# Performance work log

Hardware: AMD Instinct MI355X
Metric: run time of the kernel (lower is better)

Reference implementation:

```python
import jax, jax.numpy as jnp
import numpy as np

EPS = 1e-7
LN_EPS = 1e-6


def project(x):
    norm = jnp.maximum(jnp.linalg.norm(x, axis=-1, keepdims=True), EPS)
    max_norm = 1.0 - EPS
    return jnp.where(norm >= 1.0, x / norm * max_norm, x)


def mobius_add(x, y, c):
    x2 = jnp.sum(x * x, -1, keepdims=True)
    y2 = jnp.sum(y * y, -1, keepdims=True)
    xy = jnp.sum(x * y, -1, keepdims=True)
    num = (1 + 2 * c * xy + c * y2) * x + (1 - c * x2) * y
    den = 1 + 2 * c * xy + c * c * x2 * y2
    return project(num / jnp.maximum(den, EPS))


def logmap0(y, c):
    sqrt_c = jnp.maximum(jnp.sqrt(c), EPS)
    y_norm = jnp.linalg.norm(y, axis=-1, keepdims=True)
    safe = jnp.maximum(y_norm, EPS)
    mag = jnp.arctanh(jnp.minimum(y_norm, 1.0 - EPS)) / sqrt_c
    return jnp.where(y_norm < EPS, jnp.zeros_like(y), mag * (y / safe))


def expmap0(v, c):
    sqrt_c = jnp.maximum(jnp.sqrt(c), EPS)
    v_norm = jnp.linalg.norm(v, axis=-1, keepdims=True)
    safe = jnp.maximum(v_norm, EPS)
    mag = jnp.tanh(sqrt_c * safe) / sqrt_c
    return project(jnp.where(v_norm < EPS, jnp.zeros_like(v), mag * (v / safe)))


def poincare_dist(x, y, c):
    # x: [B,H,N,1,D], y: [B,H,N,W,D], c: [B,1,1,1,1] -> dist [B,H,N,W]
    sqrt_c = jnp.maximum(jnp.sqrt(c), EPS)
    add_norm = jnp.linalg.norm(mobius_add(-x, y, c), axis=-1)
    arg = jnp.minimum(sqrt_c.squeeze(-1) * add_norm, 1.0 - EPS)
    return 2.0 * jnp.arctanh(arg) / sqrt_c.squeeze(-1)


def sliding_windows(x, window):
    # x: [B,H,N,Dh] -> [B,H,N,window,Dh] of the last `window` keys per query (zero-padded)
    B, H, N, Dh = x.shape
    pad = jnp.zeros((B, H, window - 1, Dh), dtype=x.dtype)
    xp = jnp.concatenate([pad, x], axis=2)
    idx = jnp.arange(window)[None, :] + jnp.arange(N)[:, None]  # [N, W]
    return xp[:, :, idx, :]


def layer_norm(x, scale, bias):
    mu = jnp.mean(x, axis=-1, keepdims=True)
    var = jnp.mean(jnp.square(x - mu), axis=-1, keepdims=True)
    return (x - mu) * jax.lax.rsqrt(var + LN_EPS) * scale + bias


def setup_inputs() -> dict:
    key = jax.random.key(0)
    B, N, DIM, H = 2, 1024, 1024, 16
    Dh = DIM // H
    ks = jax.random.split(key, 16)
    s = 1.0 / np.sqrt(DIM)
    x = 0.01 * jax.random.normal(ks[0], (B, N, DIM), jnp.float32)  # well inside the ball
    # rotary angles: pos * inv_freq, shape [N, Dh//2]
    inv_freq = 1.0 / (10000.0 ** (np.arange(0, Dh // 2, dtype=np.float32) * 2.0 / Dh))
    freqs = jnp.asarray(np.arange(N, dtype=np.float32)[:, None] * inv_freq[None, :])
    c = 0.5 + 0.5 * jax.random.uniform(ks[1], (B,), jnp.float32)
    p = {
        'Wq': s * jax.random.normal(ks[2], (DIM, DIM), jnp.float32), 'bq': jnp.zeros((DIM,), jnp.float32),
        'Wk': s * jax.random.normal(ks[3], (DIM, DIM), jnp.float32), 'bk': jnp.zeros((DIM,), jnp.float32),
        'Wv': s * jax.random.normal(ks[4], (DIM, DIM), jnp.float32), 'bv': jnp.zeros((DIM,), jnp.float32),
        'Wo': s * jax.random.normal(ks[5], (DIM, DIM), jnp.float32), 'bo': jnp.zeros((DIM,), jnp.float32),
        'W1': s * jax.random.normal(ks[6], (DIM, 4 * DIM), jnp.float32), 'b1': jnp.zeros((4 * DIM,), jnp.float32),
        'W2': (1.0 / np.sqrt(4 * DIM)) * jax.random.normal(ks[7], (4 * DIM, DIM), jnp.float32), 'b2': jnp.zeros((DIM,), jnp.float32),
        'ln1_scale': jnp.ones((DIM,), jnp.float32), 'ln1_bias': jnp.zeros((DIM,), jnp.float32),
        'ln2_scale': jnp.ones((DIM,), jnp.float32), 'ln2_bias': jnp.zeros((DIM,), jnp.float32),
        'geo_scale': jnp.ones((H, 1, 1), jnp.float32),
    }
    return dict(x=x, freqs=freqs, c=c, **p)


def reference(x, freqs, c, Wq, bq, Wk, bk, Wv, bv, Wo, bo, W1, b1, W2, b2,
              ln1_scale, ln1_bias, ln2_scale, ln2_bias, geo_scale):
    WINDOW = 32
    B, N, DIM = x.shape
    H = geo_scale.shape[0]
    Dh = DIM // H
    c_ln = c.reshape(B, 1, 1)
    c_attn = c.reshape(B, 1, 1, 1)
    c_d = c.reshape(B, 1, 1, 1, 1)

    # tangent-space layer norm 1
    x_norm = expmap0(layer_norm(logmap0(x, c_ln), ln1_scale, ln1_bias), c_ln)
    x_tan = logmap0(x_norm, c_ln)

    q = (x_tan @ Wq + bq).reshape(B, N, H, Dh)
    k = (x_tan @ Wk + bk).reshape(B, N, H, Dh)
    v = (x_tan @ Wv + bv).reshape(B, N, H, Dh)

    # rotary embedding (real-arithmetic form of complex multiply)
    cos = jnp.cos(freqs).reshape(1, N, 1, Dh // 2)
    sin = jnp.sin(freqs).reshape(1, N, 1, Dh // 2)

    def rope(t):
        t_r, t_i = jnp.split(t, 2, -1)
        return jnp.concatenate([t_r * cos - t_i * sin, t_r * sin + t_i * cos], -1)

    q_hyp = expmap0(rope(q), c_attn)
    k_hyp = expmap0(rope(k), c_attn)

    q_t = q_hyp.transpose(0, 2, 1, 3)  # [B,H,N,Dh]
    k_t = k_hyp.transpose(0, 2, 1, 3)
    v_t = v.transpose(0, 2, 1, 3)

    k_w = sliding_windows(k_t, WINDOW)  # [B,H,N,W,Dh]
    v_w = sliding_windows(v_t, WINDOW)

    dist = poincare_dist(q_t[:, :, :, None, :], k_w, c_d)  # [B,H,N,W]
    attn = jax.nn.softmax(-geo_scale * dist, axis=-1)
    attn_out = jnp.einsum('bhnw,bhnwd->bhnd', attn, v_w).transpose(0, 2, 1, 3).reshape(B, N, DIM)

    attn_hyp = expmap0(attn_out @ Wo + bo, c_ln)
    x_att = mobius_add(x, attn_hyp, c_ln)

    # tangent-space layer norm 2 + hyperbolic FFN
    x_norm2 = expmap0(layer_norm(logmap0(x_att, c_ln), ln2_scale, ln2_bias), c_ln)
    t = logmap0(x_norm2, c_ln)
    ffn_tan = jax.nn.gelu(t @ W1 + b1) @ W2 + b2
    x_ffn = expmap0(ffn_tan, c_ln)
    return mobius_add(x_att, x_ffn, c_ln)
```

## Files before the change

### kernel.cpp

```cpp
#include <hip/hip_runtime.h>
#include <cmath>

static constexpr int SEQ = 1024;
static constexpr int DIM = 1024;
static constexpr int NH  = 16;
static constexpr int DH  = 64;
static constexpr int WB  = 2;
static constexpr int ROWS = WB * SEQ;
__device__ static constexpr double D_EPS = 1e-7;

typedef __attribute__((ext_vector_type(8))) short short8v;
typedef __attribute__((ext_vector_type(4))) float float4v;

__device__ __forceinline__ uint32_t bf16_hi_bits(float f) {
  uint32_t u = __float_as_uint(f);
  return (u + 0x7fffu + ((u >> 16) & 1u)) >> 16;
}
__device__ __forceinline__ uint32_t pack_hl(float f) {
  const uint32_t h = bf16_hi_bits(f);
  const float fh = __uint_as_float(h << 16);
  const uint32_t l = bf16_hi_bits(f - fh);
  return h | (l << 16);
}

__device__ __forceinline__ double wsum64(double v) {
#pragma unroll
  for (int m = 32; m >= 1; m >>= 1) v += __shfl_xor(v, m, 64);
  return v;
}

__global__ __launch_bounds__(256) void ln_tan_kernel(
    const float* __restrict__ xin, const float* __restrict__ cb,
    const float* __restrict__ gamma, const float* __restrict__ beta,
    uint32_t* __restrict__ out) {
  __shared__ double sh[2][4];
  const int row = blockIdx.x;
  const int b = row / SEQ;
  const float* xr = xin + (size_t)row * DIM;
  const int t = threadIdx.x;
  float xv[4];
  double s0 = 0.0, s1 = 0.0;
#pragma unroll
  for (int i = 0; i < 4; i++) {
    xv[i] = xr[t + 256 * i];
    s0 += (double)xv[i];
    s1 += (double)xv[i] * (double)xv[i];
  }
  s0 = wsum64(s0); s1 = wsum64(s1);
  const int wid = t >> 6, lane = t & 63;
  if (lane == 0) { sh[0][wid] = s0; sh[1][wid] = s1; }
  __syncthreads();
  s0 = sh[0][0] + sh[0][1] + sh[0][2] + sh[0][3];
  s1 = sh[1][0] + sh[1][1] + sh[1][2] + sh[1][3];

  const double cc  = (double)cb[b];
  const double sqc = fmax(sqrt(cc), D_EPS);
  const double xn  = sqrt(s1);
  double a = 0.0;
  if (xn >= D_EPS) a = atanh(fmin(xn, 1.0 - D_EPS)) / sqc / fmax(xn, D_EPS);
  const double mu   = a * s0 / (double)DIM;
  const double var  = a * a * s1 / (double)DIM - mu * mu;
  const double invs = 1.0 / sqrt(var + 1e-6);

  double tv[4]; double s2 = 0.0;
#pragma unroll
  for (int i = 0; i < 4; i++) {
    const int col = t + 256 * i;
    tv[i] = (a * (double)xv[i] - mu) * invs * (double)gamma[col] + (double)beta[col];
    s2 += tv[i] * tv[i];
  }
  s2 = wsum64(s2);
  __syncthreads();
  if (lane == 0) sh[0][wid] = s2;
  __syncthreads();
  s2 = sh[0][0] + sh[0][1] + sh[0][2] + sh[0][3];

  const double tn = sqrt(s2);
  double C = 0.0;
  if (tn >= D_EPS) {
    const double safe_t = fmax(tn, D_EPS);
    const double mag2 = tanh(sqc * safe_t) / sqc;
    const double en = mag2 * (tn / safe_t);
    const double pn = fmax(en, D_EPS);
    const double f  = (pn >= 1.0) ? (1.0 - D_EPS) / pn : 1.0;
    const double yn = en * f;
    if (yn >= D_EPS) {
      const double mag3 = atanh(fmin(yn, 1.0 - D_EPS)) / sqc;
      C = (mag2 / safe_t) * f * (mag3 / fmax(yn, D_EPS));
    }
  }
  uint32_t* orow = out + (size_t)row * DIM;
#pragma unroll
  for (int i = 0; i < 4; i++) orow[t + 256 * i] = pack_hl((float)(tv[i] * C));
}

__global__ __launch_bounds__(256) void expmobius_parts4_kernel(
    const float* __restrict__ xb, const float* __restrict__ parts,
    const float* __restrict__ bias, const float* __restrict__ cb,
    float* __restrict__ out) {
  __shared__ double sh[3][4];
  const size_t PSZ = (size_t)ROWS * DIM;
  const int row = blockIdx.x;
  const int b = row / SEQ;
  const float* xr = xb + (size_t)row * DIM;
  const float* p0r = parts + (size_t)row * DIM;
  const int t = threadIdx.x;
  float xv[4];
  double tv[4];
  double sx2 = 0.0, st2 = 0.0, sxt = 0.0;
#pragma unroll
  for (int i = 0; i < 4; i++) {
    const int col = t + 256 * i;
    xv[i] = xr[col];
    tv[i] = (double)p0r[col] + (double)p0r[col + PSZ] +
            (double)p0r[col + 2 * PSZ] + (double)p0r[col + 3 * PSZ] +
            (double)bias[col];
    sx2 += (double)xv[i] * (double)xv[i];
    st2 += tv[i] * tv[i];
    sxt += (double)xv[i] * tv[i];
  }
  sx2 = wsum64(sx2); st2 = wsum64(st2); sxt = wsum64(sxt);
  const int wid = t >> 6, lane = t & 63;
  if (lane == 0) { sh[0][wid] = sx2; sh[1][wid] = st2; sh[2][wid] = sxt; }
  __syncthreads();
  sx2 = sh[0][0] + sh[0][1] + sh[0][2] + sh[0][3];
  st2 = sh[1][0] + sh[1][1] + sh[1][2] + sh[1][3];
  sxt = sh[2][0] + sh[2][1] + sh[2][2] + sh[2][3];

  const double cc  = (double)cb[b];
  const double sqc = fmax(sqrt(cc), D_EPS);
  const double tn = sqrt(st2);
  double s = 0.0;
  if (tn >= D_EPS) {
    const double safe = fmax(tn, D_EPS);
    const double mag = tanh(sqc * safe) / sqc;
    const double en = mag * (tn / safe);
    const double pn = fmax(en, D_EPS);
    const double f  = (pn >= 1.0) ? (1.0 - D_EPS) / pn : 1.0;
    s = (mag / safe) * f;
  }
  const double x2 = sx2, y2 = s * s * st2, xy = s * sxt;
  const double P   = 1.0 + 2.0 * cc * xy + cc * y2;
  const double Q   = 1.0 - cc * x2;
  const double den = fmax(1.0 + 2.0 * cc * xy + cc * cc * x2 * y2, D_EPS);
  const double num2 = P * P * x2 + Q * Q * y2 + 2.0 * P * Q * xy;
  const double rn  = sqrt(fmax(num2, 0.0)) / den;
  const double pn2 = fmax(rn, D_EPS);
  const double pf  = (pn2 >= 1.0) ? (1.0 - D_EPS) / pn2 : 1.0;
  const double Pd = (P / den) * pf;
  const double Qd = (Q / den) * pf * s;
  float* orow = out + (size_t)row * DIM;
#pragma unroll
  for (int i = 0; i < 4; i++)
    orow[t + 256 * i] = (float)(Pd * (double)xv[i] + Qd * tv[i]);
}

__global__ __launch_bounds__(256) void rope_expmap_kernel(
    float* __restrict__ q, float* __restrict__ k,
    const float* __restrict__ freqs, const float* __restrict__ cb) {
  const int row = blockIdx.x;
  const int b = row / SEQ, n = row % SEQ;
  const int t = threadIdx.x;
  const int h = t >> 4, j = t & 15;
  const int p1 = j, p2 = j + 16;
  const double f1 = (double)freqs[n * (DH / 2) + p1];
  const double f2 = (double)freqs[n * (DH / 2) + p2];
  const double c1 = cos(f1), s1 = sin(f1);
  const double c2 = cos(f2), s2 = sin(f2);
  const double cc  = (double)cb[b];
  const double sqc = fmax(sqrt(cc), D_EPS);
  const size_t base = (size_t)row * DIM + (size_t)h * DH;
  float* arrs[2] = {q, k};
#pragma unroll
  for (int a = 0; a < 2; a++) {
    float* p = arrs[a] + base;
    const double xr1 = p[p1], xi1 = p[p1 + 32];
    const double xr2 = p[p2], xi2 = p[p2 + 32];
    const double r1 = xr1 * c1 - xi1 * s1, i1 = xr1 * s1 + xi1 * c1;
    const double r2 = xr2 * c2 - xi2 * s2, i2 = xr2 * s2 + xi2 * c2;
    double nrm2 = r1 * r1 + i1 * i1 + r2 * r2 + i2 * i2;
#pragma unroll
    for (int m = 8; m >= 1; m >>= 1) nrm2 += __shfl_xor(nrm2, m, 16);
    const double vn = sqrt(nrm2);
    double sc = 0.0;
    if (vn >= D_EPS) {
      const double safe = fmax(vn, D_EPS);
      const double mag = tanh(sqc * safe) / sqc;
      const double en = mag * (vn / safe);
      const double pn = fmax(en, D_EPS);
      const double f  = (pn >= 1.0) ? (1.0 - D_EPS) / pn : 1.0;
      sc = (mag / safe) * f;
    }
    p[p1] = (float)(r1 * sc); p[p1 + 32] = (float)(i1 * sc);
    p[p2] = (float)(r2 * sc); p[p2 + 32] = (float)(i2 * sc);
  }
}

__global__ __launch_bounds__(256) void attn_kernel(
    const float* __restrict__ qh, const float* __restrict__ kh,
    const float* __restrict__ v, const float* __restrict__ cb,
    const float* __restrict__ geo, uint32_t* __restrict__ out) {
  __shared__ float qs[8][DH];
  const int g = threadIdx.x >> 5;
  const int w = threadIdx.x & 31;
  const int gid = blockIdx.x * 8 + g;
  const int n = gid & (SEQ - 1);
  const int bh = gid >> 10;
  const int h = bh & (NH - 1);
  const int b = bh >> 4;
  const size_t qbase = ((size_t)(b * SEQ + n)) * DIM + (size_t)h * DH;
  qs[g][w] = qh[qbase + w];
  qs[g][w + 32] = qh[qbase + w + 32];
  __syncthreads();

  const double cc  = (double)cb[b];
  const double sqc = fmax(sqrt(cc), D_EPS);
  double q2p = (double)qs[g][w] * qs[g][w] + (double)qs[g][w + 32] * qs[g][w + 32];
#pragma unroll
  for (int m = 16; m >= 1; m >>= 1) q2p += __shfl_xor(q2p, m, 32);
  const double a2 = q2p;

  const int msrc = n - 31 + w;
  double y2 = 0.0, qy = 0.0;
  if (msrc >= 0) {
    const float* kr = kh + ((size_t)(b * SEQ + msrc)) * DIM + (size_t)h * DH;
#pragma unroll 8
    for (int d = 0; d < DH; d++) {
      const double kv = (double)kr[d];
      y2 += kv * kv;
      qy += (double)qs[g][d] * kv;
    }
  }
  const double ay = -qy;
  const double P = 1.0 + 2.0 * cc * ay + cc * y2;
  const double Q = 1.0 - cc * a2;
  const double den = fmax(1.0 + 2.0 * cc * ay + cc * cc * a2 * y2, D_EPS);
  const double num2 = P * P * a2 + Q * Q * y2 + 2.0 * P * Q * ay;
  const double rn = sqrt(fmax(num2, 0.0)) / den;
  const double pn = fmax(rn, D_EPS);
  const double addn = (pn >= 1.0) ? (1.0 - D_EPS) * (rn / pn) : rn;
  const double arg = fmin(sqc * addn, 1.0 - D_EPS);
  const double dist = 2.0 * atanh(arg) / sqc;
  const double logit = -(double)geo[h] * dist;

  double mx = logit;
#pragma unroll
  for (int m = 16; m >= 1; m >>= 1) mx = fmax(mx, __shfl_xor(mx, m, 32));
  const double e = exp(logit - mx);
  double se = e;
#pragma unroll
  for (int m = 16; m >= 1; m >>= 1) se += __shfl_xor(se, m, 32);
  const double p = e / se;

  double acc1 = 0.0, acc2 = 0.0;
  for (int wp = 0; wp < 32; wp++) {
    const double pw = __shfl(p, wp, 32);
    const int mp = n - 31 + wp;
    if (mp >= 0) {
      const float* vr = v + ((size_t)(b * SEQ + mp)) * DIM + (size_t)h * DH;
      acc1 += pw * (double)vr[w];
      acc2 += pw * (double)vr[w + 32];
    }
  }
  out[qbase + w] = pack_hl((float)acc1);
  out[qbase + w + 32] = pack_hl((float)acc2);
}

__device__ __forceinline__ float gelu_tanh(float x) {
  const float x3 = x * x * x;
  return 0.5f * x * (1.0f + tanhf(0.7978845608028654f * (x + 0.044715f * x3)));
}

template <int EPI>
__device__ __forceinline__ void mfma_gemm_body(
    const uint32_t* __restrict__ Ap, int Kld,
    const float* __restrict__ Wf, const float* __restrict__ bias,
    void* __restrict__ Cout, int N, int k0, int klen, int m0, int n0) {
  __shared__ __align__(16) short AsH[4096], AsL[4096], BsH[4096], BsL[4096];
  const int t = threadIdx.x;
  const int lane = t & 63, wave = t >> 6;
  const int wm = (wave >> 1) << 6, wn = (wave & 1) << 6;
  const int am = t >> 1, akh = (t & 1) << 4;
  const uint32_t* Ag = Ap + (size_t)(m0 + am) * Kld + k0 + akh;
  const int as_ = am >> 4, ai = am & 15, aq0 = akh >> 3;
  short* awH0 = &AsH[((as_ << 6) + (aq0 << 4) + ai) << 3];
  short* awH1 = &AsH[((as_ << 6) + ((aq0 + 1) << 4) + ai) << 3];
  short* awL0 = &AsL[((as_ << 6) + (aq0 << 4) + ai) << 3];
  short* awL1 = &AsL[((as_ << 6) + ((aq0 + 1) << 4) + ai) << 3];
  const int bn = t & 127, bkg = (t >> 7) << 4;
  const float* Bg = Wf + (size_t)(k0 + bkg) * N + n0 + bn;
  const int bs = bn >> 4, bi = bn & 15, bq0 = bkg >> 3;
  short* bwH0 = &BsH[((bs << 6) + (bq0 << 4) + bi) << 3];
  short* bwH1 = &BsH[((bs << 6) + ((bq0 + 1) << 4) + bi) << 3];
  short* bwL0 = &BsL[((bs << 6) + (bq0 << 4) + bi) << 3];
  short* bwL1 = &BsL[((bs << 6) + ((bq0 + 1) << 4) + bi) << 3];

  float4v acc[4][4];
#pragma unroll
  for (int i = 0; i < 4; i++)
#pragma unroll
    for (int j = 0; j < 4; j++) acc[i][j] = (float4v){0.f, 0.f, 0.f, 0.f};

  uint32_t a[16];
  float bf[16];
  {
    const uint4* p = (const uint4*)Ag;
#pragma unroll
    for (int r = 0; r < 4; r++) { uint4 u = p[r]; a[4*r] = u.x; a[4*r+1] = u.y; a[4*r+2] = u.z; a[4*r+3] = u.w; }
#pragma unroll
    for (int r = 0; r < 16; r++) bf[r] = Bg[(size_t)r * N];
  }

  for (int kt = 0; kt < klen; kt += 32) {
    __syncthreads();
    {
      uint4 h0, l0, h1, l1;
      uint32_t* hp0 = (uint32_t*)&h0; uint32_t* lp0 = (uint32_t*)&l0;
      uint32_t* hp1 = (uint32_t*)&h1; uint32_t* lp1 = (uint32_t*)&l1;
#pragma unroll
      for (int r = 0; r < 4; r++) {
        hp0[r] = (a[2*r] & 0xffffu) | (a[2*r+1] << 16);
        lp0[r] = (a[2*r] >> 16) | (a[2*r+1] & 0xffff0000u);
        hp1[r] = (a[8+2*r] & 0xffffu) | (a[8+2*r+1] << 16);
        lp1[r] = (a[8+2*r] >> 16) | (a[8+2*r+1] & 0xffff0000u);
      }
      *(uint4*)awH0 = h0; *(uint4*)awL0 = l0;
      *(uint4*)awH1 = h1; *(uint4*)awL1 = l1;
    }
    {
      uint32_t hb[16], lb[16];
#pragma unroll
      for (int r = 0; r < 16; r++) {
        const uint32_t h = bf16_hi_bits(bf[r]);
        hb[r] = h;
        lb[r] = bf16_hi_bits(bf[r] - __uint_as_float(h << 16));
      }
      uint4 h0, l0, h1, l1;
      uint32_t* hp0 = (uint32_t*)&h0; uint32_t* lp0 = (uint32_t*)&l0;
      uint32_t* hp1 = (uint32_t*)&h1; uint32_t* lp1 = (uint32_t*)&l1;
#pragma unroll
      for (int r = 0; r < 4; r++) {
        hp0[r] = hb[2*r] | (hb[2*r+1] << 16);
        lp0[r] = lb[2*r] | (lb[2*r+1] << 16);
        hp1[r] = hb[8+2*r] | (hb[8+2*r+1] << 16);
        lp1[r] = lb[8+2*r] | (lb[8+2*r+1] << 16);
      }
      *(uint4*)bwH0 = h0; *(uint4*)bwL0 = l0;
      *(uint4*)bwH1 = h1; *(uint4*)bwL1 = l1;
    }
    __syncthreads();
    {
      const int ktn = (kt + 32 < klen) ? kt + 32 : kt;
      const uint4* p = (const uint4*)(Ag + ktn);
#pragma unroll
      for (int r = 0; r < 4; r++) { uint4 u = p[r]; a[4*r] = u.x; a[4*r+1] = u.y; a[4*r+2] = u.z; a[4*r+3] = u.w; }
      const float* bp = Bg + (size_t)ktn * N;
#pragma unroll
      for (int r = 0; r < 16; r++) bf[r] = bp[(size_t)r * N];
    }
    short8v aH[4], aL[4];
    const int ams = wm >> 4;
#pragma unroll
    for (int im = 0; im < 4; im++) {
      aH[im] = *(const short8v*)&AsH[(((ams + im) << 6) + lane) << 3];
      aL[im] = *(const short8v*)&AsL[(((ams + im) << 6) + lane) << 3];
    }
    const int bns = wn >> 4;
#pragma unroll
    for (int in_ = 0; in_ < 4; in_++) {
      const short8v bH = *(const short8v*)&BsH[(((bns + in_) << 6) + lane) << 3];
      const short8v bL = *(const short8v*)&BsL[(((bns + in_) << 6) + lane) << 3];
#pragma unroll
      for (int im = 0; im < 4; im++) {
        acc[im][in_] = __builtin_amdgcn_mfma_f32_16x16x32_bf16(aH[im], bH, acc[im][in_], 0, 0, 0);
        acc[im][in_] = __builtin_amdgcn_mfma_f32_16x16x32_bf16(aH[im], bL, acc[im][in_], 0, 0, 0);
        acc[im][in_] = __builtin_amdgcn_mfma_f32_16x16x32_bf16(aL[im], bH, acc[im][in_], 0, 0, 0);
      }
    }
  }
  const int cq = lane >> 4, ci = lane & 15;
#pragma unroll
  for (int im = 0; im < 4; im++) {
    const int row = m0 + wm + im * 16 + cq * 4;
#pragma unroll
    for (int in_ = 0; in_ < 4; in_++) {
      const int col = n0 + wn + in_ * 16 + ci;
      if (EPI == 2) {
        float* C = (float*)Cout;
#pragma unroll
        for (int r = 0; r < 4; r++) C[(size_t)(row + r) * N + col] = acc[im][in_][r];
      } else {
        const float bv_ = bias[col];
        if (EPI == 0) {
          float* C = (float*)Cout;
#pragma unroll
          for (int r = 0; r < 4; r++) C[(size_t)(row + r) * N + col] = acc[im][in_][r] + bv_;
        } else {
          uint32_t* C = (uint32_t*)Cout;
#pragma unroll
          for (int r = 0; r < 4; r++)
            C[(size_t)(row + r) * N + col] = pack_hl(gelu_tanh(acc[im][in_][r] + bv_));
        }
      }
    }
  }
}

__global__ __launch_bounds__(256) void qkv_mfma(
    const uint32_t* __restrict__ Ap,
    const float* __restrict__ Wq, const float* __restrict__ bq, float* __restrict__ Cq,
    const float* __restrict__ Wk, const float* __restrict__ bk, float* __restrict__ Ck,
    const float* __restrict__ Wv, const float* __restrict__ bv, float* __restrict__ Cv) {
  const int which = blockIdx.x >> 3;
  const int n0 = (blockIdx.x & 7) << 7;
  const float* W = (which == 0) ? Wq : (which == 1) ? Wk : Wv;
  const float* bias = (which == 0) ? bq : (which == 1) ? bk : bv;
  float* C = (which == 0) ? Cq : (which == 1) ? Ck : Cv;
  mfma_gemm_body<0>(Ap, DIM, W, bias, C, DIM, 0, DIM, blockIdx.y << 7, n0);
}

__global__ __launch_bounds__(256) void ffn_up_mfma(
    const uint32_t* __restrict__ Ap, const float* __restrict__ W1,
    const float* __restrict__ b1, uint32_t* __restrict__ H) {
  mfma_gemm_body<1>(Ap, DIM, W1, b1, H, 4 * DIM, 0, DIM, blockIdx.y << 7, blockIdx.x << 7);
}

__global__ __launch_bounds__(256) void gemm_splitk_mfma(
    const uint32_t* __restrict__ Ap, int Kld, const float* __restrict__ W,
    float* __restrict__ Cbase, size_t cstride, int N, int klen) {
  mfma_gemm_body<2>(Ap, Kld, W, nullptr, Cbase + (size_t)blockIdx.z * cstride, N,
                    blockIdx.z * klen, klen, blockIdx.y << 7, blockIdx.x << 7);
}

extern "C" void kernel_launch(void* const* d_in, const int* in_sizes, int n_in,
                              void* d_out, int out_size, void* d_ws, size_t ws_size,
                              hipStream_t stream) {
  const float* x     = (const float*)d_in[0];
  const float* freqs = (const float*)d_in[1];
  const float* c     = (const float*)d_in[2];
  const float* Wq = (const float*)d_in[3];  const float* bq = (const float*)d_in[4];
  const float* Wk = (const float*)d_in[5];  const float* bk = (const float*)d_in[6];
  const float* Wv = (const float*)d_in[7];  const float* bv = (const float*)d_in[8];
  const float* Wo = (const float*)d_in[9];  const float* bo = (const float*)d_in[10];
  const float* W1 = (const float*)d_in[11]; const float* b1 = (const float*)d_in[12];
  const float* W2 = (const float*)d_in[13]; const float* b2 = (const float*)d_in[14];
  const float* g1 = (const float*)d_in[15]; const float* be1 = (const float*)d_in[16];
  const float* g2 = (const float*)d_in[17]; const float* be2 = (const float*)d_in[18];
  const float* geo = (const float*)d_in[19];
  float* out = (float*)d_out;
  float* ws = (float*)d_ws;

  const size_t SZ = (size_t)ROWS * DIM;
  uint32_t* x_tanP = (uint32_t*)(ws + 0 * SZ);
  float*    qb     = ws + 1 * SZ;
  float*    kb     = ws + 2 * SZ;
  float*    vb     = ws + 3 * SZ;
  uint32_t* attP   = (uint32_t*)(ws + 4 * SZ);
  float*    x_att  = ws + 5 * SZ;
  uint32_t* h1P    = (uint32_t*)(ws + 6 * SZ);
  float*    woP    = ws + 0 * SZ;
  float*    fdP    = ws + 1 * SZ;
  uint32_t* t2P    = (uint32_t*)(ws + 0 * SZ);

  ln_tan_kernel<<<ROWS, 256, 0, stream>>>(x, c, g1, be1, x_tanP);
  qkv_mfma<<<dim3(24, ROWS / 128), 256, 0, stream>>>(
      x_tanP, Wq, bq, qb, Wk, bk, kb, Wv, bv, vb);
  rope_expmap_kernel<<<ROWS, 256, 0, stream>>>(qb, kb, freqs, c);
  attn_kernel<<<WB * NH * SEQ / 8, 256, 0, stream>>>(qb, kb, vb, c, geo, attP);
  gemm_splitk_mfma<<<dim3(DIM / 128, ROWS / 128, 4), 256, 0, stream>>>(
      attP, DIM, Wo, woP, SZ, DIM, DIM / 4);
  expmobius_parts4_kernel<<<ROWS, 256, 0, stream>>>(x, woP, bo, c, x_att);
  ln_tan_kernel<<<ROWS, 256, 0, stream>>>(x_att, c, g2, be2, t2P);
  ffn_up_mfma<<<dim3(4 * DIM / 128, ROWS / 128), 256, 0, stream>>>(t2P, W1, b1, h1P);
  gemm_splitk_mfma<<<dim3(DIM / 128, ROWS / 128, 4), 256, 0, stream>>>(
      h1P, 4 * DIM, W2, fdP, SZ, DIM, DIM);
  expmobius_parts4_kernel<<<ROWS, 256, 0, stream>>>(x_att, fdP, b2, c, out);
  (void)in_sizes; (void)n_in; (void)out_size; (void)ws_size;
}
```

Before: 461.9 us.

## Pre-split operands into tiled hi/lo bf16 planes for direct GEMM tile loads

Weights are now converted once per call by a new kernel into separate hi/lo bf16 planes, stored in a tile-major layout that matches the shared-memory MFMA tiles. Activation producers (layer norm, attention, FFN up) write the same tiled hi/lo layout. The GEMM main loop can then copy contiguous uint4 chunks straight into LDS, with no per-tile fp32-to-bf16 splitting or strided weight loads. The cost is extra weight-conversion launches, scattered 2-byte stores from the producers, and more workspace reuse, including writing x_att into the output buffer.

```diff
diff --git a/kernel.cpp b/kernel.cpp
--- a/kernel.cpp
+++ b/kernel.cpp
@@ -9,6 +9,7 @@
 static constexpr int ROWS = WB * SEQ;
 __device__ static constexpr double D_EPS = 1e-7;
 
+typedef unsigned short ushort_t;
 typedef __attribute__((ext_vector_type(8))) short short8v;
 typedef __attribute__((ext_vector_type(4))) float float4v;
 
@@ -16,23 +17,53 @@
   uint32_t u = __float_as_uint(f);
   return (u + 0x7fffu + ((u >> 16) & 1u)) >> 16;
 }
-__device__ __forceinline__ uint32_t pack_hl(float f) {
-  const uint32_t h = bf16_hi_bits(f);
-  const float fh = __uint_as_float(h << 16);
-  const uint32_t l = bf16_hi_bits(f - fh);
-  return h | (l << 16);
+
+__device__ __forceinline__ size_t tiled_addr(int row, int col, int Kld) {
+  return ((size_t)(row >> 7) * (Kld >> 5) + (col >> 5)) * 4096
+       + (size_t)((((row >> 4) & 7) << 9) + (((col >> 3) & 3) << 7) + ((row & 15) << 3) + (col & 7));
+}
+__device__ __forceinline__ void store_hl(ushort_t* __restrict__ hi, ushort_t* __restrict__ lo,
+                                         size_t addr, float f) {
+  const uint32_t hb = bf16_hi_bits(f);
+  hi[addr] = (ushort_t)hb;
+  lo[addr] = (ushort_t)bf16_hi_bits(f - __uint_as_float(hb << 16));
 }
 
 __device__ __forceinline__ double wsum64(double v) {
 #pragma unroll
   for (int m = 32; m >= 1; m >>= 1) v += __shfl_xor(v, m, 64);
   return v;
+}
+
+__global__ __launch_bounds__(256) void conv_w_kernel(
+    const float* __restrict__ W, ushort_t* __restrict__ hi, ushort_t* __restrict__ lo,
+    int K, int N) {
+  const int tid = blockIdx.x * 256 + threadIdx.x;
+  const int n = tid % N;
+  const int k0 = (tid / N) << 3;
+  uint32_t hw[4], lw[4];
+#pragma unroll
+  for (int rp = 0; rp < 4; rp++) {
+    uint32_t h2[2], l2[2];
+#pragma unroll
+    for (int e = 0; e < 2; e++) {
+      const float f = W[(size_t)(k0 + rp * 2 + e) * N + n];
+      const uint32_t hb = bf16_hi_bits(f);
+      h2[e] = hb;
+      l2[e] = bf16_hi_bits(f - __uint_as_float(hb << 16));
+    }
+    hw[rp] = h2[0] | (h2[1] << 16);
+    lw[rp] = l2[0] | (l2[1] << 16);
+  }
+  const size_t addr = tiled_addr(n, k0, K);
+  *(uint4*)&hi[addr] = *(uint4*)hw;
+  *(uint4*)&lo[addr] = *(uint4*)lw;
 }
 
 __global__ __launch_bounds__(256) void ln_tan_kernel(
     const float* __restrict__ xin, const float* __restrict__ cb,
     const float* __restrict__ gamma, const float* __restrict__ beta,
-    uint32_t* __restrict__ out) {
+    ushort_t* __restrict__ ohi, ushort_t* __restrict__ olo) {
   __shared__ double sh[2][4];
   const int row = blockIdx.x;
   const int b = row / SEQ;
@@ -89,21 +120,23 @@
       C = (mag2 / safe_t) * f * (mag3 / fmax(yn, D_EPS));
     }
   }
-  uint32_t* orow = out + (size_t)row * DIM;
-#pragma unroll
-  for (int i = 0; i < 4; i++) orow[t + 256 * i] = pack_hl((float)(tv[i] * C));
+#pragma unroll
+  for (int i = 0; i < 4; i++) {
+    const int col = t + 256 * i;
+    store_hl(ohi, olo, tiled_addr(row, col, DIM), (float)(tv[i] * C));
+  }
 }
 
 __global__ __launch_bounds__(256) void expmobius_parts4_kernel(
-    const float* __restrict__ xb, const float* __restrict__ parts,
+    const float* __restrict__ xb,
+    const float* __restrict__ p0, const float* __restrict__ p1,
+    const float* __restrict__ p2, const float* __restrict__ p3,
     const float* __restrict__ bias, const float* __restrict__ cb,
     float* __restrict__ out) {
   __shared__ double sh[3][4];
-  const size_t PSZ = (size_t)ROWS * DIM;
   const int row = blockIdx.x;
   const int b = row / SEQ;
-  const float* xr = xb + (size_t)row * DIM;
-  const float* p0r = parts + (size_t)row * DIM;
+  const size_t ro = (size_t)row * DIM;
   const int t = threadIdx.x;
   float xv[4];
   double tv[4];
@@ -111,10 +144,9 @@
 #pragma unroll
   for (int i = 0; i < 4; i++) {
     const int col = t + 256 * i;
-    xv[i] = xr[col];
-    tv[i] = (double)p0r[col] + (double)p0r[col + PSZ] +
-            (double)p0r[col + 2 * PSZ] + (double)p0r[col + 3 * PSZ] +
-            (double)bias[col];
+    xv[i] = xb[ro + col];
+    tv[i] = (double)p0[ro + col] + (double)p1[ro + col] +
+            (double)p2[ro + col] + (double)p3[ro + col] + (double)bias[col];
     sx2 += (double)xv[i] * (double)xv[i];
     st2 += tv[i] * tv[i];
     sxt += (double)xv[i] * tv[i];
@@ -149,10 +181,9 @@
   const double pf  = (pn2 >= 1.0) ? (1.0 - D_EPS) / pn2 : 1.0;
   const double Pd = (P / den) * pf;
   const double Qd = (Q / den) * pf * s;
-  float* orow = out + (size_t)row * DIM;
 #pragma unroll
   for (int i = 0; i < 4; i++)
-    orow[t + 256 * i] = (float)(Pd * (double)xv[i] + Qd * tv[i]);
+    out[ro + t + 256 * i] = (float)(Pd * (double)xv[i] + Qd * tv[i]);
 }
 
 __global__ __launch_bounds__(256) void rope_expmap_kernel(
@@ -199,7 +230,8 @@
 __global__ __launch_bounds__(256) void attn_kernel(
     const float* __restrict__ qh, const float* __restrict__ kh,
     const float* __restrict__ v, const float* __restrict__ cb,
-    const float* __restrict__ geo, uint32_t* __restrict__ out) {
+    const float* __restrict__ geo,
+    ushort_t* __restrict__ ohi, ushort_t* __restrict__ olo) {
   __shared__ float qs[8][DH];
   const int g = threadIdx.x >> 5;
   const int w = threadIdx.x & 31;
@@ -208,7 +240,8 @@
   const int bh = gid >> 10;
   const int h = bh & (NH - 1);
   const int b = bh >> 4;
-  const size_t qbase = ((size_t)(b * SEQ + n)) * DIM + (size_t)h * DH;
+  const int row = b * SEQ + n;
+  const size_t qbase = (size_t)row * DIM + (size_t)h * DH;
   qs[g][w] = qh[qbase + w];
   qs[g][w + 32] = qh[qbase + w + 32];
   __syncthreads();
@@ -262,8 +295,9 @@
       acc2 += pw * (double)vr[w + 32];
     }
   }
-  out[qbase + w] = pack_hl((float)acc1);
-  out[qbase + w + 32] = pack_hl((float)acc2);
+  const int col = h * DH + w;
+  store_hl(ohi, olo, tiled_addr(row, col, DIM), (float)acc1);
+  store_hl(ohi, olo, tiled_addr(row, col + 32, DIM), (float)acc2);
 }
 
 __device__ __forceinline__ float gelu_tanh(float x) {
@@ -273,27 +307,17 @@
 
 template <int EPI>
 __device__ __forceinline__ void mfma_gemm_body(
-    const uint32_t* __restrict__ Ap, int Kld,
-    const float* __restrict__ Wf, const float* __restrict__ bias,
-    void* __restrict__ Cout, int N, int k0, int klen, int m0, int n0) {
+    const ushort_t* __restrict__ Ahi, const ushort_t* __restrict__ Alo, int Kld,
+    const ushort_t* __restrict__ Bhi, const ushort_t* __restrict__ Blo, int KB,
+    const float* __restrict__ bias, float* __restrict__ Cf,
+    ushort_t* __restrict__ Chi, ushort_t* __restrict__ Clo, int KldOut,
+    int N, int k0, int klen, int m0, int n0) {
   __shared__ __align__(16) short AsH[4096], AsL[4096], BsH[4096], BsL[4096];
   const int t = threadIdx.x;
   const int lane = t & 63, wave = t >> 6;
   const int wm = (wave >> 1) << 6, wn = (wave & 1) << 6;
-  const int am = t >> 1, akh = (t & 1) << 4;
-  const uint32_t* Ag = Ap + (size_t)(m0 + am) * Kld + k0 + akh;
-  const int as_ = am >> 4, ai = am & 15, aq0 = akh >> 3;
-  short* awH0 = &AsH[((as_ << 6) + (aq0 << 4) + ai) << 3];
-  short* awH1 = &AsH[((as_ << 6) + ((aq0 + 1) << 4) + ai) << 3];
-  short* awL0 = &AsL[((as_ << 6) + (aq0 << 4) + ai) << 3];
-  short* awL1 = &AsL[((as_ << 6) + ((aq0 + 1) << 4) + ai) << 3];
-  const int bn = t & 127, bkg = (t >> 7) << 4;
-  const float* Bg = Wf + (size_t)(k0 + bkg) * N + n0 + bn;
-  const int bs = bn >> 4, bi = bn & 15, bq0 = bkg >> 3;
-  short* bwH0 = &BsH[((bs << 6) + (bq0 << 4) + bi) << 3];
-  short* bwH1 = &BsH[((bs << 6) + ((bq0 + 1) << 4) + bi) << 3];
-  short* bwL0 = &BsL[((bs << 6) + (bq0 << 4) + bi) << 3];
-  short* bwL1 = &BsL[((bs << 6) + ((bq0 + 1) << 4) + bi) << 3];
+  const size_t abase = (size_t)(m0 >> 7) * (Kld >> 5) * 4096;
+  const size_t bbase = (size_t)(n0 >> 7) * (KB >> 5) * 4096;
 
   float4v acc[4][4];
 #pragma unroll
@@ -301,62 +325,31 @@
 #pragma unroll
     for (int j = 0; j < 4; j++) acc[i][j] = (float4v){0.f, 0.f, 0.f, 0.f};
 
-  uint32_t a[16];
-  float bf[16];
+  uint4 rah0, rah1, ral0, ral1, rbh0, rbh1, rbl0, rbl1;
   {
-    const uint4* p = (const uint4*)Ag;
-#pragma unroll
-    for (int r = 0; r < 4; r++) { uint4 u = p[r]; a[4*r] = u.x; a[4*r+1] = u.y; a[4*r+2] = u.z; a[4*r+3] = u.w; }
-#pragma unroll
-    for (int r = 0; r < 16; r++) bf[r] = Bg[(size_t)r * N];
+    const size_t at = abase + (size_t)(k0 >> 5) * 4096;
+    const size_t bt = bbase + (size_t)(k0 >> 5) * 4096;
+    rah0 = ((const uint4*)(Ahi + at))[t]; rah1 = ((const uint4*)(Ahi + at))[t + 256];
+    ral0 = ((const uint4*)(Alo + at))[t]; ral1 = ((const uint4*)(Alo + at))[t + 256];
+    rbh0 = ((const uint4*)(Bhi + bt))[t]; rbh1 = ((const uint4*)(Bhi + bt))[t + 256];
+    rbl0 = ((const uint4*)(Blo + bt))[t]; rbl1 = ((const uint4*)(Blo + bt))[t + 256];
   }
 
   for (int kt = 0; kt < klen; kt += 32) {
     __syncthreads();
-    {
-      uint4 h0, l0, h1, l1;
-      uint32_t* hp0 = (uint32_t*)&h0; uint32_t* lp0 = (uint32_t*)&l0;
-      uint32_t* hp1 = (uint32_t*)&h1; uint32_t* lp1 = (uint32_t*)&l1;
-#pragma unroll
-      for (int r = 0; r < 4; r++) {
-        hp0[r] = (a[2*r] & 0xffffu) | (a[2*r+1] << 16);
-        lp0[r] = (a[2*r] >> 16) | (a[2*r+1] & 0xffff0000u);
-        hp1[r] = (a[8+2*r] & 0xffffu) | (a[8+2*r+1] << 16);
-        lp1[r] = (a[8+2*r] >> 16) | (a[8+2*r+1] & 0xffff0000u);
-      }
-      *(uint4*)awH0 = h0; *(uint4*)awL0 = l0;
-      *(uint4*)awH1 = h1; *(uint4*)awL1 = l1;
-    }
-    {
-      uint32_t hb[16], lb[16];
-#pragma unroll
-      for (int r = 0; r < 16; r++) {
-        const uint32_t h = bf16_hi_bits(bf[r]);
-        hb[r] = h;
-        lb[r] = bf16_hi_bits(bf[r] - __uint_as_float(h << 16));
-      }
-      uint4 h0, l0, h1, l1;
-      uint32_t* hp0 = (uint32_t*)&h0; uint32_t* lp0 = (uint32_t*)&l0;
-      uint32_t* hp1 = (uint32_t*)&h1; uint32_t* lp1 = (uint32_t*)&l1;
-#pragma unroll
-      for (int r = 0; r < 4; r++) {
-        hp0[r] = hb[2*r] | (hb[2*r+1] << 16);
-        lp0[r] = lb[2*r] | (lb[2*r+1] << 16);
-        hp1[r] = hb[8+2*r] | (hb[8+2*r+1] << 16);
-        lp1[r] = lb[8+2*r] | (lb[8+2*r+1] << 16);
-      }
-      *(uint4*)bwH0 = h0; *(uint4*)bwL0 = l0;
-      *(uint4*)bwH1 = h1; *(uint4*)bwL1 = l1;
-    }
+    ((uint4*)AsH)[t] = rah0; ((uint4*)AsH)[t + 256] = rah1;
+    ((uint4*)AsL)[t] = ral0; ((uint4*)AsL)[t + 256] = ral1;
+    ((uint4*)BsH)[t] = rbh0; ((uint4*)BsH)[t + 256] = rbh1;
+    ((uint4*)BsL)[t] = rbl0; ((uint4*)BsL)[t + 256] = rbl1;
     __syncthreads();
     {
       const int ktn = (kt + 32 < klen) ? kt + 32 : kt;
-      const uint4* p = (const uint4*)(Ag + ktn);
-#pragma unroll
-      for (int r = 0; r < 4; r++) { uint4 u = p[r]; a[4*r] = u.x; a[4*r+1] = u.y; a[4*r+2] = u.z; a[4*r+3] = u.w; }
-      const float* bp = Bg + (size_t)ktn * N;
-#pragma unroll
-      for (int r = 0; r < 16; r++) bf[r] = bp[(size_t)r * N];
+      const size_t at = abase + (size_t)((k0 + ktn) >> 5) * 4096;
+      const size_t bt = bbase + (size_t)((k0 + ktn) >> 5) * 4096;
+      rah0 = ((const uint4*)(Ahi + at))[t]; rah1 = ((const uint4*)(Ahi + at))[t + 256];
+      ral0 = ((const uint4*)(Alo + at))[t]; ral1 = ((const uint4*)(Alo + at))[t + 256];
+      rbh0 = ((const uint4*)(Bhi + bt))[t]; rbh1 = ((const uint4*)(Bhi + bt))[t + 256];
+      rbl0 = ((const uint4*)(Blo + bt))[t]; rbl1 = ((const uint4*)(Blo + bt))[t + 256];
     }
     short8v aH[4], aL[4];
     const int ams = wm >> 4;
@@ -386,50 +379,54 @@
     for (int in_ = 0; in_ < 4; in_++) {
       const int col = n0 + wn + in_ * 16 + ci;
       if (EPI == 2) {
-        float* C = (float*)Cout;
-#pragma unroll
-        for (int r = 0; r < 4; r++) C[(size_t)(row + r) * N + col] = acc[im][in_][r];
+#pragma unroll
+        for (int r = 0; r < 4; r++) Cf[(size_t)(row + r) * N + col] = acc[im][in_][r];
+      } else if (EPI == 0) {
+        const float bv_ = bias[col];
+#pragma unroll
+        for (int r = 0; r < 4; r++) Cf[(size_t)(row + r) * N + col] = acc[im][in_][r] + bv_;
       } else {
         const float bv_ = bias[col];
-        if (EPI == 0) {
-          float* C = (float*)Cout;
-#pragma unroll
-          for (int r = 0; r < 4; r++) C[(size_t)(row + r) * N + col] = acc[im][in_][r] + bv_;
-        } else {
-          uint32_t* C = (uint32_t*)Cout;
-#pragma unroll
-          for (int r = 0; r < 4; r++)
-            C[(size_t)(row + r) * N + col] = pack_hl(gelu_tanh(acc[im][in_][r] + bv_));
-        }
+#pragma unroll
+        for (int r = 0; r < 4; r++)
+          store_hl(Chi, Clo, tiled_addr(row + r, col, KldOut),
+                   gelu_tanh(acc[im][in_][r] + bv_));
       }
     }
   }
 }
 
 __global__ __launch_bounds__(256) void qkv_mfma(
-    const uint32_t* __restrict__ Ap,
-    const float* __restrict__ Wq, const float* __restrict__ bq, float* __restrict__ Cq,
-    const float* __restrict__ Wk, const float* __restrict__ bk, float* __restrict__ Ck,
-    const float* __restrict__ Wv, const float* __restrict__ bv, float* __restrict__ Cv) {
+    const ushort_t* __restrict__ Ahi, const ushort_t* __restrict__ Alo,
+    const ushort_t* __restrict__ Whi, const ushort_t* __restrict__ Wlo,
+    const float* __restrict__ bq, const float* __restrict__ bk, const float* __restrict__ bv,
+    float* __restrict__ Cq, float* __restrict__ Ck, float* __restrict__ Cv) {
   const int which = blockIdx.x >> 3;
   const int n0 = (blockIdx.x & 7) << 7;
-  const float* W = (which == 0) ? Wq : (which == 1) ? Wk : Wv;
+  const size_t woff = (size_t)which * (1u << 20);
   const float* bias = (which == 0) ? bq : (which == 1) ? bk : bv;
   float* C = (which == 0) ? Cq : (which == 1) ? Ck : Cv;
-  mfma_gemm_body<0>(Ap, DIM, W, bias, C, DIM, 0, DIM, blockIdx.y << 7, n0);
+  mfma_gemm_body<0>(Ahi, Alo, DIM, Whi + woff, Wlo + woff, DIM, bias, C,
+                    nullptr, nullptr, 0, DIM, 0, DIM, blockIdx.y << 7, n0);
 }
 
 __global__ __launch_bounds__(256) void ffn_up_mfma(
-    const uint32_t* __restrict__ Ap, const float* __restrict__ W1,
-    const float* __restrict__ b1, uint32_t* __restrict__ H) {
-  mfma_gemm_body<1>(Ap, DIM, W1, b1, H, 4 * DIM, 0, DIM, blockIdx.y << 7, blockIdx.x << 7);
+    const ushort_t* __restrict__ Ahi, const ushort_t* __restrict__ Alo,
+    const ushort_t* __restrict__ W1hi, const ushort_t* __restrict__ W1lo,
+    const float* __restrict__ b1, ushort_t* __restrict__ Hhi, ushort_t* __restrict__ Hlo) {
+  mfma_gemm_body<1>(Ahi, Alo, DIM, W1hi, W1lo, DIM, b1, nullptr, Hhi, Hlo, 4 * DIM,
+                    4 * DIM, 0, DIM, blockIdx.y << 7, blockIdx.x << 7);
 }
 
 __global__ __launch_bounds__(256) void gemm_splitk_mfma(
-    const uint32_t* __restrict__ Ap, int Kld, const float* __restrict__ W,
-    float* __restrict__ Cbase, size_t cstride, int N, int klen) {
-  mfma_gemm_body<2>(Ap, Kld, W, nullptr, Cbase + (size_t)blockIdx.z * cstride, N,
-                    blockIdx.z * klen, klen, blockIdx.y << 7, blockIdx.x << 7);
+    const ushort_t* __restrict__ Ahi, const ushort_t* __restrict__ Alo, int Kld,
+    const ushort_t* __restrict__ Bhi, const ushort_t* __restrict__ Blo, int KB,
+    float* __restrict__ C0, float* __restrict__ C1,
+    float* __restrict__ C2, float* __restrict__ C3, int N, int klen) {
+  const int z = blockIdx.z;
+  float* C = (z == 0) ? C0 : (z == 1) ? C1 : (z == 2) ? C2 : C3;
+  mfma_gemm_body<2>(Ahi, Alo, Kld, Bhi, Blo, KB, nullptr, C, nullptr, nullptr, 0,
+                    N, z * klen, klen, blockIdx.y << 7, blockIdx.x << 7);
 }
 
 extern "C" void kernel_launch(void* const* d_in, const int* in_sizes, int n_in,
@@ -451,29 +448,43 @@
   float* ws = (float*)d_ws;
 
   const size_t SZ = (size_t)ROWS * DIM;
-  uint32_t* x_tanP = (uint32_t*)(ws + 0 * SZ);
-  float*    qb     = ws + 1 * SZ;
-  float*    kb     = ws + 2 * SZ;
-  float*    vb     = ws + 3 * SZ;
-  uint32_t* attP   = (uint32_t*)(ws + 4 * SZ);
-  float*    x_att  = ws + 5 * SZ;
-  uint32_t* h1P    = (uint32_t*)(ws + 6 * SZ);
-  float*    woP    = ws + 0 * SZ;
-  float*    fdP    = ws + 1 * SZ;
-  uint32_t* t2P    = (uint32_t*)(ws + 0 * SZ);
-
-  ln_tan_kernel<<<ROWS, 256, 0, stream>>>(x, c, g1, be1, x_tanP);
+  const size_t PL = SZ;
+  const uint32_t M1 = 1u << 20;
+  auto us = [&](int i) { return (ushort_t*)(ws + (size_t)i * SZ); };
+
+  ushort_t* xt_hi = us(0);           ushort_t* xt_lo = us(0) + PL;
+  float* qb = ws + 1 * SZ; float* kb = ws + 2 * SZ; float* vb = ws + 3 * SZ;
+  ushort_t* at_hi = us(4);           ushort_t* at_lo = us(4) + PL;
+  ushort_t* qkvo_hi = us(5);         ushort_t* qkvo_lo = us(6);
+  ushort_t* w1_hi = us(7);           ushort_t* w1_lo = us(8);
+  ushort_t* w2_hi = us(5);           ushort_t* w2_lo = us(6);
+  ushort_t* t2_hi = us(4);           ushort_t* t2_lo = us(4) + PL;
+  ushort_t* h1_hi = us(0);           ushort_t* h1_lo = us(2);
+  float* x_att = out;
+
+  conv_w_kernel<<<512, 256, 0, stream>>>(Wq, qkvo_hi + 0 * M1, qkvo_lo + 0 * M1, DIM, DIM);
+  conv_w_kernel<<<512, 256, 0, stream>>>(Wk, qkvo_hi + 1 * M1, qkvo_lo + 1 * M1, DIM, DIM);
+  conv_w_kernel<<<512, 256, 0, stream>>>(Wv, qkvo_hi + 2 * M1, qkvo_lo + 2 * M1, DIM, DIM);
+  conv_w_kernel<<<512, 256, 0, stream>>>(Wo, qkvo_hi + 3 * M1, qkvo_lo + 3 * M1, DIM, DIM);
+  conv_w_kernel<<<2048, 256, 0, stream>>>(W1, w1_hi, w1_lo, DIM, 4 * DIM);
+  ln_tan_kernel<<<ROWS, 256, 0, stream>>>(x, c, g1, be1, xt_hi, xt_lo);
   qkv_mfma<<<dim3(24, ROWS / 128), 256, 0, stream>>>(
-      x_tanP, Wq, bq, qb, Wk, bk, kb, Wv, bv, vb);
+      xt_hi, xt_lo, qkvo_hi, qkvo_lo, bq, bk, bv, qb, kb, vb);
   rope_expmap_kernel<<<ROWS, 256, 0, stream>>>(qb, kb, freqs, c);
-  attn_kernel<<<WB * NH * SEQ / 8, 256, 0, stream>>>(qb, kb, vb, c, geo, attP);
+  attn_kernel<<<WB * NH * SEQ / 8, 256, 0, stream>>>(qb, kb, vb, c, geo, at_hi, at_lo);
   gemm_splitk_mfma<<<dim3(DIM / 128, ROWS / 128, 4), 256, 0, stream>>>(
-      attP, DIM, Wo, woP, SZ, DIM, DIM / 4);
-  expmobius_parts4_kernel<<<ROWS, 256, 0, stream>>>(x, woP, bo, c, x_att);
-  ln_tan_kernel<<<ROWS, 256, 0, stream>>>(x_att, c, g2, be2, t2P);
-  ffn_up_mfma<<<dim3(4 * DIM / 128, ROWS / 128), 256, 0, stream>>>(t2P, W1, b1, h1P);
+      at_hi, at_lo, DIM, qkvo_hi + 3 * M1, qkvo_lo + 3 * M1, DIM,
+      ws + 0 * SZ, ws + 1 * SZ, ws + 2 * SZ, ws + 3 * SZ, DIM, DIM / 4);
+  conv_w_kernel<<<2048, 256, 0, stream>>>(W2, w2_hi, w2_lo, 4 * DIM, DIM);
+  expmobius_parts4_kernel<<<ROWS, 256, 0, stream>>>(
+      x, ws + 0 * SZ, ws + 1 * SZ, ws + 2 * SZ, ws + 3 * SZ, bo, c, x_att);
+  ln_tan_kernel<<<ROWS, 256, 0, stream>>>(x_att, c, g2, be2, t2_hi, t2_lo);
+  ffn_up_mfma<<<dim3(4 * DIM / 128, ROWS / 128), 256, 0, stream>>>(
+      t2_hi, t2_lo, w1_hi, w1_lo, b1, h1_hi, h1_lo);
   gemm_splitk_mfma<<<dim3(DIM / 128, ROWS / 128, 4), 256, 0, stream>>>(
-      h1P, 4 * DIM, W2, fdP, SZ, DIM, DIM);
-  expmobius_parts4_kernel<<<ROWS, 256, 0, stream>>>(x_att, fdP, b2, c, out);
+      h1_hi, h1_lo, 4 * DIM, w2_hi, w2_lo, 4 * DIM,
+      ws + 4 * SZ, ws + 7 * SZ, ws + 8 * SZ, ws + 9 * SZ, DIM, DIM);
+  expmobius_parts4_kernel<<<ROWS, 256, 0, stream>>>(
+      x_att, ws + 4 * SZ, ws + 7 * SZ, ws + 8 * SZ, ws + 9 * SZ, b2, c, out);
   (void)in_sizes; (void)n_in; (void)out_size; (void)ws_size;
 }
```

Result: faster. 430.6 us (-6.8%).
